# Performance work log

Measured on AMD Instinct MI355X. Metric: run time of the kernel, lower is better.

## Reference

```python
import jax, jax.numpy as jnp
import numpy as np

GNO_RADIUS = 0.1
SCALES = (1.0, 2.0)


def _rescale(x):
    # rescale coords per batch/dim to [-1, 1] (matches repo's rescale())
    mn = x.min(axis=1, keepdims=True)
    mx = x.max(axis=1, keepdims=True)
    return 2.0 * (x - mn) / (mx - mn + 1e-12) - 1.0


def setup_inputs() -> dict:
    key = jax.random.key(0)
    ks = jax.random.split(key, 6)
    B, N, M, Din, C, D, H = 2, 1024, 1024, 16, 32, 2, 32
    pndata = jax.random.normal(ks[0], (B, N, Din), dtype=jnp.float32)
    x_coord = jax.random.uniform(ks[1], (B, N, D), dtype=jnp.float32)
    # latent queries: regular 32x32 grid in [-1,1]^2 (regional node positions)
    g = jnp.linspace(-1.0, 1.0, 32, dtype=jnp.float32)
    latent_queries = jnp.stack(jnp.meshgrid(g, g, indexing='ij'), axis=-1).reshape(M, D)
    # lifting ChannelMLP (1 layer == pointwise linear)
    W_lift = jax.random.normal(ks[2], (Din, C), dtype=jnp.float32) / np.sqrt(Din)
    b_lift = jnp.zeros((C,), dtype=jnp.float32)
    # IntegralTransform kernel MLP: [2*D -> H -> C], gelu between layers
    W1 = jax.random.normal(ks[3], (2 * D, H), dtype=jnp.float32) / np.sqrt(2 * D)
    b1 = jnp.zeros((H,), dtype=jnp.float32)
    W2 = jax.random.normal(ks[4], (H, C), dtype=jnp.float32) / np.sqrt(H)
    b2 = jnp.zeros((C,), dtype=jnp.float32)
    return dict(pndata=pndata, x_coord=x_coord, latent_queries=latent_queries,
                W_lift=W_lift, b_lift=b_lift, W1=W1, b1=b1, W2=W2, b2=b2)


def reference(pndata, x_coord, latent_queries, W_lift, b_lift, W1, b1, W2, b2):
    # pndata: [B,N,Din], x_coord: [B,N,D], latent_queries: [M,D]
    x = _rescale(x_coord)                           # [B,N,D]
    f = pndata @ W_lift + b_lift                    # lifting -> [B,N,C]
    q = latent_queries                              # [M,D]
    B, N, D = x.shape
    M = q.shape[0]
    # squared distances query->point: [B,M,N]
    d2 = jnp.sum((q[None, :, None, :] - x[:, None, :, :]) ** 2, axis=-1)
    # kernel MLP input: concat(y_j, x_i) per (query i, point j): [B,M,N,2D]
    feat = jnp.concatenate([
        jnp.broadcast_to(x[:, None, :, :], (B, M, N, D)),
        jnp.broadcast_to(q[None, :, None, :], (B, M, N, D)),
    ], axis=-1)
    k = jax.nn.gelu(feat @ W1 + b1) @ W2 + b2       # [B,M,N,C]
    kv = k * f[:, None, :, :]                       # 'linear' transform: k(x,y) * f(y)
    out = jnp.zeros((B, M, kv.shape[-1]), dtype=kv.dtype)
    for s in SCALES:                                # small fixed scale set
        mask = (d2 <= (GNO_RADIUS * s) ** 2).astype(kv.dtype)   # radius-ball neighbors
        cnt = jnp.maximum(mask.sum(axis=-1), 1.0)               # [B,M]
        agg = jnp.einsum('bmn,bmnc->bmc', mask, kv) / cnt[..., None]  # mean reduce
        out = out + agg                              # sum over scales
    return out
```

## Files before the change

### kernel.cpp

```cpp
#include <hip/hip_runtime.h>

#define BB 2
#define NN 1024
#define MM 1024
#define DIN 16
#define CC 32
#define HH 32

__device__ __forceinline__ float gelu_tanh(float v) {
    float v3 = v * v * v;
    float u = 0.7978845608028654f * (v + 0.044715f * v3);
    float e = __expf(2.0f * u);
    float t = 1.0f - 2.0f * __builtin_amdgcn_rcpf(e + 1.0f);
    return 0.5f * v * (1.0f + t);
}

__global__ __launch_bounds__(256) void gno_fused(
    const float* __restrict__ pndata, const float* __restrict__ x_coord,
    const float* __restrict__ latq,
    const float* __restrict__ W_lift, const float* __restrict__ b_lift,
    const float* __restrict__ W1, const float* __restrict__ b1,
    const float* __restrict__ W2, const float* __restrict__ b2,
    float* __restrict__ out)
{
    const int bid = blockIdx.x;
    const int b = bid >> 9;
    const int ipair = bid & 511;
    const int i0 = ipair * 2;
    const int t = threadIdx.x;
    const int lane = t & 63;
    const int wave = t >> 6;
    const int g = t >> 5;
    const int c = t & 31;
    const int qi = g >> 2;
    const int sg = g & 3;

    __shared__ float2 xs[NN];
    __shared__ unsigned meta[2][NN];
    __shared__ __align__(16) float hbuf[8 * HH];
    __shared__ float accs[8 * CC];
    __shared__ float redf[16];
    __shared__ int kcnt[2][4];
    __shared__ int k1cnt[2][4];

    const float w1a = W1[c];
    const float w1b = W1[HH + c];
    const float w1c = W1[2 * HH + c];
    const float w1d = W1[3 * HH + c];
    const float b1v = b1[c];
    const float b2v = b2[c];
    const float blv = b_lift[c];
    float wl[DIN];
    #pragma unroll
    for (int k = 0; k < DIN; ++k) wl[k] = W_lift[k * CC + c];
    float w2c[HH];
    #pragma unroll
    for (int h = 0; h < HH; ++h) w2c[h] = W2[h * CC + c];

    const float4 qq = *((const float4*)&latq[2 * i0]);

    const float2* xcb = (const float2*)x_coord + b * NN;
    float2 xyc[4];
    float mn0 = 1e30f, mx0 = -1e30f, mn1 = 1e30f, mx1 = -1e30f;
    #pragma unroll
    for (int kk = 0; kk < 4; ++kk) {
        xyc[kk] = xcb[wave * 256 + kk * 64 + lane];
        mn0 = fminf(mn0, xyc[kk].x); mx0 = fmaxf(mx0, xyc[kk].x);
        mn1 = fminf(mn1, xyc[kk].y); mx1 = fmaxf(mx1, xyc[kk].y);
    }
    #pragma unroll
    for (int off = 32; off > 0; off >>= 1) {
        mn0 = fminf(mn0, __shfl_down(mn0, off));
        mx0 = fmaxf(mx0, __shfl_down(mx0, off));
        mn1 = fminf(mn1, __shfl_down(mn1, off));
        mx1 = fmaxf(mx1, __shfl_down(mx1, off));
    }
    if (lane == 0) {
        redf[wave * 4 + 0] = mn0; redf[wave * 4 + 1] = mx0;
        redf[wave * 4 + 2] = mn1; redf[wave * 4 + 3] = mx1;
    }
    __syncthreads();
    const float Amn0 = fminf(fminf(redf[0], redf[4]),  fminf(redf[8],  redf[12]));
    const float Amx0 = fmaxf(fmaxf(redf[1], redf[5]),  fmaxf(redf[9],  redf[13]));
    const float Amn1 = fminf(fminf(redf[2], redf[6]),  fminf(redf[10], redf[14]));
    const float Amx1 = fmaxf(fmaxf(redf[3], redf[7]),  fmaxf(redf[11], redf[15]));
    const float den0 = __fadd_rn(__fsub_rn(Amx0, Amn0), 1e-12f);
    const float den1 = __fadd_rn(__fsub_rn(Amx1, Amn1), 1e-12f);

    const float t1 = 0.01f;
    const float t2 = 0.04f;

    const unsigned long long lmask = (1ull << lane) - 1ull;
    int kw0 = 0, k1w0 = 0, kw1 = 0, k1w1 = 0;
    #pragma unroll
    for (int kk = 0; kk < 4; ++kk) {
        const int j = wave * 256 + kk * 64 + lane;
        float r0 = __fsub_rn(__fdiv_rn(__fmul_rn(2.0f, __fsub_rn(xyc[kk].x, Amn0)), den0), 1.0f);
        float r1 = __fsub_rn(__fdiv_rn(__fmul_rn(2.0f, __fsub_rn(xyc[kk].y, Amn1)), den1), 1.0f);
        xs[j] = make_float2(r0, r1);
        {
            float dx = __fsub_rn(qq.x, r0);
            float dy = __fsub_rn(qq.y, r1);
            float d2 = __fadd_rn(__fmul_rn(dx, dx), __fmul_rn(dy, dy));
            bool h2 = d2 <= t2, h1 = d2 <= t1;
            unsigned long long m2 = __ballot(h2);
            unsigned long long m1 = __ballot(h1);
            if (h2) meta[0][wave * 256 + kw0 + __popcll(m2 & lmask)] =
                        (unsigned)j | (h1 ? 1024u : 0u);
            kw0 += (int)__popcll(m2);
            k1w0 += (int)__popcll(m1);
        }
        {
            float dx = __fsub_rn(qq.z, r0);
            float dy = __fsub_rn(qq.w, r1);
            float d2 = __fadd_rn(__fmul_rn(dx, dx), __fmul_rn(dy, dy));
            bool h2 = d2 <= t2, h1 = d2 <= t1;
            unsigned long long m2 = __ballot(h2);
            unsigned long long m1 = __ballot(h1);
            if (h2) meta[1][wave * 256 + kw1 + __popcll(m2 & lmask)] =
                        (unsigned)j | (h1 ? 1024u : 0u);
            kw1 += (int)__popcll(m2);
            k1w1 += (int)__popcll(m1);
        }
    }
    if (lane == 0) {
        kcnt[0][wave] = kw0; k1cnt[0][wave] = k1w0;
        kcnt[1][wave] = kw1; k1cnt[1][wave] = k1w1;
    }
    __syncthreads();

    const int Ks0 = kcnt[qi][0], Ks1 = kcnt[qi][1], Ks2 = kcnt[qi][2], Ks3 = kcnt[qi][3];
    const int K2 = Ks0 + Ks1 + Ks2 + Ks3;
    const int c1 = k1cnt[qi][0] + k1cnt[qi][1] + k1cnt[qi][2] + k1cnt[qi][3];
    const float inv1 = 1.0f / fmaxf((float)c1, 1.0f);
    const float inv2 = 1.0f / fmaxf((float)K2, 1.0f);
    const float qx = qi ? qq.z : qq.x;
    const float qy = qi ? qq.w : qq.y;
    const float ci = fmaf(qy, w1d, fmaf(qx, w1c, b1v));

    float acc = 0.0f;
    #pragma unroll
    for (int seg = 0; seg < 4; ++seg) {
        const int Ks = (seg == 0) ? Ks0 : (seg == 1) ? Ks1 : (seg == 2) ? Ks2 : Ks3;
        const int base = seg * 256;
        const int nt = (Ks + 3) >> 2;
        for (int it = 0; it < nt; ++it) {
            const int ib = it * 4 + sg;
            const bool active = ib < Ks;
            const unsigned m = meta[qi][base + (active ? ib : 0)];
            const int j = (int)(m & 1023u);
            const float w = ((m & 1024u) ? inv1 : 0.0f) + inv2;

            const float4* pd4 = (const float4*)&pndata[(b * NN + j) * DIN];
            float4 pA = pd4[0], pB = pd4[1], pC = pd4[2], pD = pd4[3];

            const float2 xy = xs[j];
            float pre = fmaf(xy.y, w1b, fmaf(xy.x, w1a, ci));
            hbuf[g * HH + c] = gelu_tanh(pre);

            float p0 = b2v, p1 = 0.0f, p2 = 0.0f, p3 = 0.0f;
            const float4* hb4 = (const float4*)&hbuf[g * HH];
            #pragma unroll
            for (int hh = 0; hh < 2; ++hh) {
                float4 h0 = hb4[hh],     h1v = hb4[hh + 2],
                       h2v = hb4[hh + 4], h3v = hb4[hh + 6];
                p0 = fmaf(h0.x,  w2c[4*hh + 0],  p0); p0 = fmaf(h0.y,  w2c[4*hh + 1],  p0);
                p0 = fmaf(h0.z,  w2c[4*hh + 2],  p0); p0 = fmaf(h0.w,  w2c[4*hh + 3],  p0);
                p1 = fmaf(h1v.x, w2c[4*hh + 8],  p1); p1 = fmaf(h1v.y, w2c[4*hh + 9],  p1);
                p1 = fmaf(h1v.z, w2c[4*hh + 10], p1); p1 = fmaf(h1v.w, w2c[4*hh + 11], p1);
                p2 = fmaf(h2v.x, w2c[4*hh + 16], p2); p2 = fmaf(h2v.y, w2c[4*hh + 17], p2);
                p2 = fmaf(h2v.z, w2c[4*hh + 18], p2); p2 = fmaf(h2v.w, w2c[4*hh + 19], p2);
                p3 = fmaf(h3v.x, w2c[4*hh + 24], p3); p3 = fmaf(h3v.y, w2c[4*hh + 25], p3);
                p3 = fmaf(h3v.z, w2c[4*hh + 26], p3); p3 = fmaf(h3v.w, w2c[4*hh + 27], p3);
            }
            float kc = (p0 + p1) + (p2 + p3);

            float f0 = blv, f1 = 0.0f;
            f0 = fmaf(pA.x, wl[0],  f0); f1 = fmaf(pA.y, wl[1],  f1);
            f0 = fmaf(pA.z, wl[2],  f0); f1 = fmaf(pA.w, wl[3],  f1);
            f0 = fmaf(pB.x, wl[4],  f0); f1 = fmaf(pB.y, wl[5],  f1);
            f0 = fmaf(pB.z, wl[6],  f0); f1 = fmaf(pB.w, wl[7],  f1);
            f0 = fmaf(pC.x, wl[8],  f0); f1 = fmaf(pC.y, wl[9],  f1);
            f0 = fmaf(pC.z, wl[10], f0); f1 = fmaf(pC.w, wl[11], f1);
            f0 = fmaf(pD.x, wl[12], f0); f1 = fmaf(pD.y, wl[13], f1);
            f0 = fmaf(pD.z, wl[14], f0); f1 = fmaf(pD.w, wl[15], f1);
            float fv = f0 + f1;

            if (active) acc = fmaf(w, kc * fv, acc);
        }
    }
    accs[g * CC + c] = acc;
    __syncthreads();
    if (t < 64) {
        const int q2 = t >> 5;
        const int cc = t & 31;
        float s = (accs[(q2 * 4 + 0) * CC + cc] + accs[(q2 * 4 + 1) * CC + cc]) +
                  (accs[(q2 * 4 + 2) * CC + cc] + accs[(q2 * 4 + 3) * CC + cc]);
        out[(b * MM + i0 + q2) * CC + cc] = s;
    }
}

extern "C" void kernel_launch(void* const* d_in, const int* in_sizes, int n_in,
                              void* d_out, int out_size, void* d_ws, size_t ws_size,
                              hipStream_t stream) {
    const float* pndata = (const float*)d_in[0];
    const float* x_coord = (const float*)d_in[1];
    const float* latq = (const float*)d_in[2];
    const float* W_lift = (const float*)d_in[3];
    const float* b_lift = (const float*)d_in[4];
    const float* W1 = (const float*)d_in[5];
    const float* b1 = (const float*)d_in[6];
    const float* W2 = (const float*)d_in[7];
    const float* b2 = (const float*)d_in[8];
    float* out = (float*)d_out;

    gno_fused<<<BB * MM / 2, 256, 0, stream>>>(pndata, x_coord, latq,
                                               W_lift, b_lift, W1, b1, W2, b2, out);
}
```

Measured before the change: 18.66 us.

## Compact neighbor list globally and software-pipeline the gelu/hbuf stage

Neighbor compaction now runs as two passes: the first counts hits per wave, the second writes indices at global prefix offsets. This gives each query one contiguous list instead of four per-wave segments, so the per-segment loop with its tail waste is replaced by a single loop over all neighbors. The main loop double-buffers hbuf and computes the next neighbor's gelu hidden values while the current one's W2 dot product runs. Launch bounds now request 4 blocks per SM. The cost is an extra barrier and ballot pass, plus register pressure from prefetched state under the occupancy hint.

```diff
diff --git a/kernel.cpp b/kernel.cpp
--- a/kernel.cpp
+++ b/kernel.cpp
@@ -15,7 +15,7 @@
     return 0.5f * v * (1.0f + t);
 }
 
-__global__ __launch_bounds__(256) void gno_fused(
+__global__ __launch_bounds__(256, 4) void gno_fused(
     const float* __restrict__ pndata, const float* __restrict__ x_coord,
     const float* __restrict__ latq,
     const float* __restrict__ W_lift, const float* __restrict__ b_lift,
@@ -25,8 +25,7 @@
 {
     const int bid = blockIdx.x;
     const int b = bid >> 9;
-    const int ipair = bid & 511;
-    const int i0 = ipair * 2;
+    const int i0 = (bid & 511) * 2;
     const int t = threadIdx.x;
     const int lane = t & 63;
     const int wave = t >> 6;
@@ -37,7 +36,7 @@
 
     __shared__ float2 xs[NN];
     __shared__ unsigned meta[2][NN];
-    __shared__ __align__(16) float hbuf[8 * HH];
+    __shared__ __align__(16) float hbuf[2][8 * HH];
     __shared__ float accs[8 * CC];
     __shared__ float redf[16];
     __shared__ int kcnt[2][4];
@@ -91,6 +90,7 @@
     const float t2 = 0.04f;
 
     const unsigned long long lmask = (1ull << lane) - 1ull;
+    unsigned bit20 = 0, bit10 = 0, bit21 = 0, bit11 = 0;
     int kw0 = 0, k1w0 = 0, kw1 = 0, k1w1 = 0;
     #pragma unroll
     for (int kk = 0; kk < 4; ++kk) {
@@ -99,28 +99,20 @@
         float r1 = __fsub_rn(__fdiv_rn(__fmul_rn(2.0f, __fsub_rn(xyc[kk].y, Amn1)), den1), 1.0f);
         xs[j] = make_float2(r0, r1);
         {
-            float dx = __fsub_rn(qq.x, r0);
-            float dy = __fsub_rn(qq.y, r1);
+            float dx = __fsub_rn(qq.x, r0), dy = __fsub_rn(qq.y, r1);
             float d2 = __fadd_rn(__fmul_rn(dx, dx), __fmul_rn(dy, dy));
             bool h2 = d2 <= t2, h1 = d2 <= t1;
-            unsigned long long m2 = __ballot(h2);
-            unsigned long long m1 = __ballot(h1);
-            if (h2) meta[0][wave * 256 + kw0 + __popcll(m2 & lmask)] =
-                        (unsigned)j | (h1 ? 1024u : 0u);
-            kw0 += (int)__popcll(m2);
-            k1w0 += (int)__popcll(m1);
-        }
-        {
-            float dx = __fsub_rn(qq.z, r0);
-            float dy = __fsub_rn(qq.w, r1);
+            bit20 |= (h2 ? 1u : 0u) << kk;  bit10 |= (h1 ? 1u : 0u) << kk;
+            kw0 += (int)__popcll(__ballot(h2));
+            k1w0 += (int)__popcll(__ballot(h1));
+        }
+        {
+            float dx = __fsub_rn(qq.z, r0), dy = __fsub_rn(qq.w, r1);
             float d2 = __fadd_rn(__fmul_rn(dx, dx), __fmul_rn(dy, dy));
             bool h2 = d2 <= t2, h1 = d2 <= t1;
-            unsigned long long m2 = __ballot(h2);
-            unsigned long long m1 = __ballot(h1);
-            if (h2) meta[1][wave * 256 + kw1 + __popcll(m2 & lmask)] =
-                        (unsigned)j | (h1 ? 1024u : 0u);
-            kw1 += (int)__popcll(m2);
-            k1w1 += (int)__popcll(m1);
+            bit21 |= (h2 ? 1u : 0u) << kk;  bit11 |= (h1 ? 1u : 0u) << kk;
+            kw1 += (int)__popcll(__ballot(h2));
+            k1w1 += (int)__popcll(__ballot(h1));
         }
     }
     if (lane == 0) {
@@ -129,64 +121,104 @@
     }
     __syncthreads();
 
-    const int Ks0 = kcnt[qi][0], Ks1 = kcnt[qi][1], Ks2 = kcnt[qi][2], Ks3 = kcnt[qi][3];
-    const int K2 = Ks0 + Ks1 + Ks2 + Ks3;
+    int base0 = 0, base1 = 0;
+    if (wave > 0) { base0 += kcnt[0][0]; base1 += kcnt[1][0]; }
+    if (wave > 1) { base0 += kcnt[0][1]; base1 += kcnt[1][1]; }
+    if (wave > 2) { base0 += kcnt[0][2]; base1 += kcnt[1][2]; }
+    #pragma unroll
+    for (int kk = 0; kk < 4; ++kk) {
+        const int j = wave * 256 + kk * 64 + lane;
+        {
+            bool h2 = (bit20 >> kk) & 1u;
+            unsigned long long m2 = __ballot(h2);
+            if (h2) meta[0][base0 + (int)__popcll(m2 & lmask)] =
+                        (unsigned)j | (((bit10 >> kk) & 1u) << 10);
+            base0 += (int)__popcll(m2);
+        }
+        {
+            bool h2 = (bit21 >> kk) & 1u;
+            unsigned long long m2 = __ballot(h2);
+            if (h2) meta[1][base1 + (int)__popcll(m2 & lmask)] =
+                        (unsigned)j | (((bit11 >> kk) & 1u) << 10);
+            base1 += (int)__popcll(m2);
+        }
+    }
+    __syncthreads();
+
+    const int K  = kcnt[qi][0] + kcnt[qi][1] + kcnt[qi][2] + kcnt[qi][3];
     const int c1 = k1cnt[qi][0] + k1cnt[qi][1] + k1cnt[qi][2] + k1cnt[qi][3];
     const float inv1 = 1.0f / fmaxf((float)c1, 1.0f);
-    const float inv2 = 1.0f / fmaxf((float)K2, 1.0f);
+    const float inv2 = 1.0f / fmaxf((float)K, 1.0f);
     const float qx = qi ? qq.z : qq.x;
     const float qy = qi ? qq.w : qq.y;
     const float ci = fmaf(qy, w1d, fmaf(qx, w1c, b1v));
 
     float acc = 0.0f;
-    #pragma unroll
-    for (int seg = 0; seg < 4; ++seg) {
-        const int Ks = (seg == 0) ? Ks0 : (seg == 1) ? Ks1 : (seg == 2) ? Ks2 : Ks3;
-        const int base = seg * 256;
-        const int nt = (Ks + 3) >> 2;
+    const int nt = (K + 3) >> 2;
+    if (nt > 0) {
+        bool act = sg < K;
+        unsigned m = meta[qi][act ? sg : 0];
+        int j = (int)(m & 1023u);
+        float wgt = ((m & 1024u) ? inv1 : 0.0f) + inv2;
+        {
+            float2 xy = xs[j];
+            float hv = gelu_tanh(fmaf(xy.y, w1b, fmaf(xy.x, w1a, ci)));
+            hbuf[0][g * HH + c] = hv;
+        }
         for (int it = 0; it < nt; ++it) {
-            const int ib = it * 4 + sg;
-            const bool active = ib < Ks;
-            const unsigned m = meta[qi][base + (active ? ib : 0)];
-            const int j = (int)(m & 1023u);
-            const float w = ((m & 1024u) ? inv1 : 0.0f) + inv2;
-
+            const int p = it & 1;
             const float4* pd4 = (const float4*)&pndata[(b * NN + j) * DIN];
-            float4 pA = pd4[0], pB = pd4[1], pC = pd4[2], pD = pd4[3];
-
-            const float2 xy = xs[j];
-            float pre = fmaf(xy.y, w1b, fmaf(xy.x, w1a, ci));
-            hbuf[g * HH + c] = gelu_tanh(pre);
+            float4 pA = pd4[0], pB4 = pd4[1], pC = pd4[2], pD = pd4[3];
+
+            const float4* hb4 = (const float4*)&hbuf[p][g * HH];
+            float4 h0 = hb4[0], h1v = hb4[1], h2v = hb4[2], h3v = hb4[3];
+            float4 h4 = hb4[4], h5v = hb4[5], h6v = hb4[6], h7v = hb4[7];
+
+            bool actn = false; unsigned mn = 0; int jn = 0; float wgtn = 0.0f;
+            if (it + 1 < nt) {
+                const int ibn = (it + 1) * 4 + sg;
+                actn = ibn < K;
+                mn = meta[qi][actn ? ibn : 0];
+                jn = (int)(mn & 1023u);
+                wgtn = ((mn & 1024u) ? inv1 : 0.0f) + inv2;
+                float2 xyn = xs[jn];
+                float hn = gelu_tanh(fmaf(xyn.y, w1b, fmaf(xyn.x, w1a, ci)));
+                hbuf[1 - p][g * HH + c] = hn;
+            }
 
             float p0 = b2v, p1 = 0.0f, p2 = 0.0f, p3 = 0.0f;
-            const float4* hb4 = (const float4*)&hbuf[g * HH];
-            #pragma unroll
-            for (int hh = 0; hh < 2; ++hh) {
-                float4 h0 = hb4[hh],     h1v = hb4[hh + 2],
-                       h2v = hb4[hh + 4], h3v = hb4[hh + 6];
-                p0 = fmaf(h0.x,  w2c[4*hh + 0],  p0); p0 = fmaf(h0.y,  w2c[4*hh + 1],  p0);
-                p0 = fmaf(h0.z,  w2c[4*hh + 2],  p0); p0 = fmaf(h0.w,  w2c[4*hh + 3],  p0);
-                p1 = fmaf(h1v.x, w2c[4*hh + 8],  p1); p1 = fmaf(h1v.y, w2c[4*hh + 9],  p1);
-                p1 = fmaf(h1v.z, w2c[4*hh + 10], p1); p1 = fmaf(h1v.w, w2c[4*hh + 11], p1);
-                p2 = fmaf(h2v.x, w2c[4*hh + 16], p2); p2 = fmaf(h2v.y, w2c[4*hh + 17], p2);
-                p2 = fmaf(h2v.z, w2c[4*hh + 18], p2); p2 = fmaf(h2v.w, w2c[4*hh + 19], p2);
-                p3 = fmaf(h3v.x, w2c[4*hh + 24], p3); p3 = fmaf(h3v.y, w2c[4*hh + 25], p3);
-                p3 = fmaf(h3v.z, w2c[4*hh + 26], p3); p3 = fmaf(h3v.w, w2c[4*hh + 27], p3);
-            }
+            p0 = fmaf(h0.x,  w2c[0],  p0); p0 = fmaf(h0.y,  w2c[1],  p0);
+            p0 = fmaf(h0.z,  w2c[2],  p0); p0 = fmaf(h0.w,  w2c[3],  p0);
+            p1 = fmaf(h1v.x, w2c[4],  p1); p1 = fmaf(h1v.y, w2c[5],  p1);
+            p1 = fmaf(h1v.z, w2c[6],  p1); p1 = fmaf(h1v.w, w2c[7],  p1);
+            p2 = fmaf(h2v.x, w2c[8],  p2); p2 = fmaf(h2v.y, w2c[9],  p2);
+            p2 = fmaf(h2v.z, w2c[10], p2); p2 = fmaf(h2v.w, w2c[11], p2);
+            p3 = fmaf(h3v.x, w2c[12], p3); p3 = fmaf(h3v.y, w2c[13], p3);
+            p3 = fmaf(h3v.z, w2c[14], p3); p3 = fmaf(h3v.w, w2c[15], p3);
+            p0 = fmaf(h4.x,  w2c[16], p0); p0 = fmaf(h4.y,  w2c[17], p0);
+            p0 = fmaf(h4.z,  w2c[18], p0); p0 = fmaf(h4.w,  w2c[19], p0);
+            p1 = fmaf(h5v.x, w2c[20], p1); p1 = fmaf(h5v.y, w2c[21], p1);
+            p1 = fmaf(h5v.z, w2c[22], p1); p1 = fmaf(h5v.w, w2c[23], p1);
+            p2 = fmaf(h6v.x, w2c[24], p2); p2 = fmaf(h6v.y, w2c[25], p2);
+            p2 = fmaf(h6v.z, w2c[26], p2); p2 = fmaf(h6v.w, w2c[27], p2);
+            p3 = fmaf(h7v.x, w2c[28], p3); p3 = fmaf(h7v.y, w2c[29], p3);
+            p3 = fmaf(h7v.z, w2c[30], p3); p3 = fmaf(h7v.w, w2c[31], p3);
             float kc = (p0 + p1) + (p2 + p3);
 
             float f0 = blv, f1 = 0.0f;
             f0 = fmaf(pA.x, wl[0],  f0); f1 = fmaf(pA.y, wl[1],  f1);
             f0 = fmaf(pA.z, wl[2],  f0); f1 = fmaf(pA.w, wl[3],  f1);
-            f0 = fmaf(pB.x, wl[4],  f0); f1 = fmaf(pB.y, wl[5],  f1);
-            f0 = fmaf(pB.z, wl[6],  f0); f1 = fmaf(pB.w, wl[7],  f1);
+            f0 = fmaf(pB4.x, wl[4], f0); f1 = fmaf(pB4.y, wl[5], f1);
+            f0 = fmaf(pB4.z, wl[6], f0); f1 = fmaf(pB4.w, wl[7], f1);
             f0 = fmaf(pC.x, wl[8],  f0); f1 = fmaf(pC.y, wl[9],  f1);
             f0 = fmaf(pC.z, wl[10], f0); f1 = fmaf(pC.w, wl[11], f1);
             f0 = fmaf(pD.x, wl[12], f0); f1 = fmaf(pD.y, wl[13], f1);
             f0 = fmaf(pD.z, wl[14], f0); f1 = fmaf(pD.w, wl[15], f1);
             float fv = f0 + f1;
 
-            if (active) acc = fmaf(w, kc * fv, acc);
+            if (act) acc = fmaf(wgt, kc * fv, acc);
+
+            act = actn; m = mn; j = jn; wgt = wgtn;
         }
     }
     accs[g * CC + c] = acc;
```

New measurement: 17.56 us, median of 2. -5.9%, faster.
